# Optimization experiments

Measured on AMD Instinct MI355X. Metric: run time of the kernel, lower is better.

## Reference

```python
import jax, jax.numpy as jnp
from jax import lax
import numpy as np

T, B, I, H = 365, 2048, 9, 50


def setup_inputs() -> dict:
    key = jax.random.key(0)
    ks = jax.random.split(key, 12)
    s = 0.1
    return {
        "x": jax.random.normal(ks[0], (T, B, I), dtype=jnp.float32),
        "w_ih0": jax.random.normal(ks[1], (4 * H, I), dtype=jnp.float32) * s,
        "w_hh0": jax.random.normal(ks[2], (4 * H, H), dtype=jnp.float32) * s,
        "b_ih0": jax.random.normal(ks[3], (4 * H,), dtype=jnp.float32) * s,
        "b_hh0": jax.random.normal(ks[4], (4 * H,), dtype=jnp.float32) * s,
        "w_ih1": jax.random.normal(ks[5], (4 * H, H), dtype=jnp.float32) * s,
        "w_hh1": jax.random.normal(ks[6], (4 * H, H), dtype=jnp.float32) * s,
        "b_ih1": jax.random.normal(ks[7], (4 * H,), dtype=jnp.float32) * s,
        "b_hh1": jax.random.normal(ks[8], (4 * H,), dtype=jnp.float32) * s,
        "fc_w": jax.random.normal(ks[9], (1, H), dtype=jnp.float32) * s,
        "fc_b": jax.random.normal(ks[10], (1,), dtype=jnp.float32) * s,
    }


def _lstm_layer(x, w_ih, w_hh, b_ih, b_hh):
    # x: [T, B, in]; PyTorch gate order: i, f, g, o
    Bq = x.shape[1]
    Hh = w_hh.shape[1]
    # precompute input projections for all timesteps (one big GEMM)
    x_proj = jnp.einsum('tbi,gi->tbg', x, w_ih) + b_ih + b_hh  # [T, B, 4H]

    def step(carry, xp):
        h, c = carry
        gates = xp + h @ w_hh.T  # [B, 4H]
        i, f, g, o = jnp.split(gates, 4, axis=-1)
        i = jax.nn.sigmoid(i)
        f = jax.nn.sigmoid(f)
        g = jnp.tanh(g)
        o = jax.nn.sigmoid(o)
        c = f * c + i * g
        h = o * jnp.tanh(c)
        return (h, c), h

    h0 = jnp.zeros((Bq, Hh), dtype=x.dtype)
    _, hs = lax.scan(step, (h0, h0), x_proj)
    return hs  # [T, B, H]


def reference(x, w_ih0, w_hh0, b_ih0, b_hh0, w_ih1, w_hh1, b_ih1, b_hh1, fc_w, fc_b):
    h1 = _lstm_layer(x, w_ih0, w_hh0, b_ih0, b_hh0)
    h2 = _lstm_layer(h1, w_ih1, w_hh1, b_ih1, b_hh1)
    out = jnp.einsum('tbh,oh->tbo', h2, fc_w) + fc_b  # [T, B, 1]
    return out
```

## Files before the change

### kernel.cpp

```cpp
#include <hip/hip_runtime.h>

#define T_STEPS 365
#define BATCH   2048
#define INP     9
#define HID     50
#define MB      16
#define NBLK    (BATCH/MB)
#define NT      896
#define NWC     13
#define L2E     1.4426950408889634f

typedef __attribute__((ext_vector_type(8))) short short8;
typedef __attribute__((ext_vector_type(4))) float float4v;

__device__ __forceinline__ unsigned f2bf(float v) {
    unsigned u = __builtin_bit_cast(unsigned, v);
    return (u + 0x7FFFu + ((u >> 16) & 1u)) >> 16;
}

#define PHASE_BARRIER() do {                                  \
    asm volatile("s_waitcnt lgkmcnt(0)" ::: "memory");        \
    __builtin_amdgcn_s_barrier();                             \
    __builtin_amdgcn_sched_barrier(0);                        \
} while (0)

__device__ __forceinline__ int hx_off(int m, int k) {
    return (m * 128 + k) ^ ((m & 7) << 3);
}

__global__ __launch_bounds__(NT, 3)
void lstm_merged(const float* __restrict__ x,
                 const float* __restrict__ w_ih0, const float* __restrict__ w_hh0,
                 const float* __restrict__ b_ih0, const float* __restrict__ b_hh0,
                 const float* __restrict__ w_ih1, const float* __restrict__ w_hh1,
                 const float* __restrict__ b_ih1, const float* __restrict__ b_hh1,
                 const float* __restrict__ fc_w, const float* __restrict__ fc_b,
                 float* __restrict__ out)
{
    __shared__ __align__(16) unsigned short HX[2][MB * 128];
    __shared__ float FCP[2][NWC][MB];

    const int tid  = threadIdx.x;
    const int w    = tid >> 6;
    const int lid  = tid & 63;
    const int mcol = lid & 15;
    const int kgrp = lid >> 4;
    const int kb8  = kgrp * 8;
    const int b0   = blockIdx.x * MB;
    const bool cw  = (w < NWC);
    const float fcb = fc_b[0];

    const int T = cw ? w : 0;
    const int r = T * 16 + mcol;
    const bool rv = cw && (r < 4 * HID);
    const int u_r = r >> 2, g_r = r & 3;
    const int orig = g_r * HID + u_r;
    const float rsc = (g_r == 2) ? (-2.f * L2E) : (-L2E);
    const int u = T * 4 + kgrp;

    short8 wk0[2], wk1[2], wk2[2];
    #pragma unroll
    for (int q = 0; q < 2; ++q) {
        short8 a{}, b{}, c{};
        #pragma unroll
        for (int j = 0; j < 8; ++j) {
            const int k = q * 32 + kb8 + j;
            float v0 = 0.f, v1 = 0.f, v2 = 0.f;
            if (rv) {
                if (k < HID) {
                    v0 = w_hh0[orig * HID + k];
                    v1 = w_ih1[orig * HID + k];
                    v2 = w_hh1[orig * HID + k];
                } else if (k < HID + INP) {
                    v0 = w_ih0[orig * INP + (k - HID)];
                }
            }
            a[j] = (short)f2bf(v0 * rsc);
            b[j] = (short)f2bf(v1 * rsc);
            c[j] = (short)f2bf(v2 * rsc);
        }
        wk0[q] = a; wk1[q] = b; wk2[q] = c;
    }
    float bs0[4], bs1[4];
    #pragma unroll
    for (int rr = 0; rr < 4; ++rr) {
        const int row = T * 16 + kgrp * 4 + rr;
        const bool bv = cw && (row < 4 * HID);
        const float bsc = (rr == 2) ? (-2.f * L2E) : (-L2E);
        bs0[rr] = bv ? (b_ih0[rr * HID + u] + b_hh0[rr * HID + u]) * bsc : 0.f;
        bs1[rr] = bv ? (b_ih1[rr * HID + u] + b_hh1[rr * HID + u]) * bsc : 0.f;
    }
    const float fcwv = (cw && u < HID) ? fc_w[u] : 0.f;
    float cst0 = 0.f, cst1 = 0.f;

    const bool xact = (!cw) && (lid < 48);
    const bool oact = (!cw) && (lid >= 48);
    const int om = lid - 48;
    float xr[3] = {0.f, 0.f, 0.f};

    for (int i = tid; i < 2 * MB * 128; i += NT) (&HX[0][0])[i] = 0;
    for (int i = tid; i < 2 * NWC * MB; i += NT) (&FCP[0][0][0])[i] = 0.f;
    __syncthreads();
    if (xact) {
        #pragma unroll
        for (int q = 0; q < 3; ++q) {
            const int xi = lid * 3 + q;
            if (xi < MB * INP) {
                const int m = xi / INP, j = xi - m * INP;
                HX[1][hx_off(m, HID + j)] =
                    (unsigned short)f2bf(x[(size_t)(b0 + m) * INP + j]);
                xr[q] = x[((size_t)BATCH + b0 + m) * INP + j];
            }
        }
    }
    __syncthreads();

    for (int ph = 0; ph <= T_STEPS + 1; ++ph) {
        const int cur = (ph + 1) & 1, nxt = ph & 1;

        if (cw) {
            const short8 f0 = *(const short8*)&HX[cur][hx_off(mcol, kb8)];
            const short8 f1 = *(const short8*)&HX[cur][hx_off(mcol, 32 + kb8)];
            const short8 f2 = *(const short8*)&HX[cur][hx_off(mcol, 64 + kb8)];
            const short8 f3 = *(const short8*)&HX[cur][hx_off(mcol, 96 + kb8)];

            if (ph < T_STEPS) {
                float4v acc = {bs0[0], bs0[1], bs0[2], bs0[3]};
                acc = __builtin_amdgcn_mfma_f32_16x16x32_bf16(wk0[0], f0, acc, 0, 0, 0);
                acc = __builtin_amdgcn_mfma_f32_16x16x32_bf16(wk0[1], f1, acc, 0, 0, 0);
                const float gi = __builtin_amdgcn_rcpf(1.f + __builtin_amdgcn_exp2f(acc[0]));
                const float gf = __builtin_amdgcn_rcpf(1.f + __builtin_amdgcn_exp2f(acc[1]));
                const float g2 = __builtin_amdgcn_rcpf(1.f + __builtin_amdgcn_exp2f(acc[2]));
                const float go = __builtin_amdgcn_rcpf(1.f + __builtin_amdgcn_exp2f(acc[3]));
                const float gg = __builtin_fmaf(2.f, g2, -1.f);
                cst0 = gf * cst0 + gi * gg;
                const float Ec = __builtin_amdgcn_exp2f(cst0 * (-2.f * L2E));
                const float tc = __builtin_fmaf(2.f, __builtin_amdgcn_rcpf(1.f + Ec), -1.f);
                const float h0v = go * tc;
                if (u < HID) HX[nxt][hx_off(mcol, u)] = (unsigned short)f2bf(h0v);
            }

            if (ph >= 1 && ph <= T_STEPS) {
                float4v accA = {bs1[0], bs1[1], bs1[2], bs1[3]};
                float4v accB = {0.f, 0.f, 0.f, 0.f};
                accA = __builtin_amdgcn_mfma_f32_16x16x32_bf16(wk1[0], f0, accA, 0, 0, 0);
                accB = __builtin_amdgcn_mfma_f32_16x16x32_bf16(wk2[0], f2, accB, 0, 0, 0);
                accA = __builtin_amdgcn_mfma_f32_16x16x32_bf16(wk1[1], f1, accA, 0, 0, 0);
                accB = __builtin_amdgcn_mfma_f32_16x16x32_bf16(wk2[1], f3, accB, 0, 0, 0);
                const float gi = __builtin_amdgcn_rcpf(1.f + __builtin_amdgcn_exp2f(accA[0] + accB[0]));
                const float gf = __builtin_amdgcn_rcpf(1.f + __builtin_amdgcn_exp2f(accA[1] + accB[1]));
                const float g2 = __builtin_amdgcn_rcpf(1.f + __builtin_amdgcn_exp2f(accA[2] + accB[2]));
                const float go = __builtin_amdgcn_rcpf(1.f + __builtin_amdgcn_exp2f(accA[3] + accB[3]));
                const float gg = __builtin_fmaf(2.f, g2, -1.f);
                cst1 = gf * cst1 + gi * gg;
                const float Ec = __builtin_amdgcn_exp2f(cst1 * (-2.f * L2E));
                const float tc = __builtin_fmaf(2.f, __builtin_amdgcn_rcpf(1.f + Ec), -1.f);
                const float h1v = go * tc;
                if (u < HID) HX[nxt][hx_off(mcol, 64 + u)] = (unsigned short)f2bf(h1v);
                float fcp = fcwv * h1v;
                fcp += __shfl_xor(fcp, 16);
                fcp += __shfl_xor(fcp, 32);
                if (lid < MB) FCP[ph & 1][w][lid] = fcp;
            }
        } else if (xact) {
            #pragma unroll
            for (int q = 0; q < 3; ++q) {
                const int xi = lid * 3 + q;
                if (xi < MB * INP) {
                    const int m = xi / INP, j = xi - m * INP;
                    float xn = 0.f;
                    if (ph + 2 < T_STEPS)
                        xn = x[((size_t)(ph + 2) * BATCH + b0 + m) * INP + j];
                    if (ph + 1 < T_STEPS)
                        HX[nxt][hx_off(m, HID + j)] = (unsigned short)f2bf(xr[q]);
                    xr[q] = xn;
                }
            }
        } else if (oact && ph >= 2) {
            const int rp = (ph - 1) & 1;
            float s = fcb;
            #pragma unroll
            for (int vv = 0; vv < NWC; ++vv) s += FCP[rp][vv][om];
            out[(size_t)(ph - 2) * BATCH + b0 + om] = s;
        }
        PHASE_BARRIER();
    }
}

extern "C" void kernel_launch(void* const* d_in, const int* in_sizes, int n_in,
                              void* d_out, int out_size, void* d_ws, size_t ws_size,
                              hipStream_t stream) {
    const float* x     = (const float*)d_in[0];
    const float* w_ih0 = (const float*)d_in[1];
    const float* w_hh0 = (const float*)d_in[2];
    const float* b_ih0 = (const float*)d_in[3];
    const float* b_hh0 = (const float*)d_in[4];
    const float* w_ih1 = (const float*)d_in[5];
    const float* w_hh1 = (const float*)d_in[6];
    const float* b_ih1 = (const float*)d_in[7];
    const float* b_hh1 = (const float*)d_in[8];
    const float* fc_w  = (const float*)d_in[9];
    const float* fc_b  = (const float*)d_in[10];
    float* out = (float*)d_out;

    lstm_merged<<<dim3(NBLK), dim3(NT), 0, stream>>>(
        x, w_ih0, w_hh0, b_ih0, b_hh0,
        w_ih1, w_hh1, b_ih1, b_hh1, fc_w, fc_b, out);
}
```

Measured before the change: 333.8 us.

## Give each compute wave two gate tiles and fold FC head into MFMA

Cuts the block from 14 to 8 waves, with each compute wave handling two of the 13 gate tiles. The FC output is folded into an otherwise unused row of the last tile's layer-1 weight matrix, which removes the FCP shared buffer and the reduction waves. It also changes the LDS layout to a k-blocked transposed form and merges the sigmoid/tanh reciprocals in the cell update. Fewer waves may make barriers cheaper, but each wave now does twice the serial work per step, and the FC output is produced in bf16 precision.

```diff
diff --git a/kernel.cpp b/kernel.cpp
--- a/kernel.cpp
+++ b/kernel.cpp
@@ -6,8 +6,9 @@
 #define HID     50
 #define MB      16
 #define NBLK    (BATCH/MB)
-#define NT      896
-#define NWC     13
+#define NT      512
+#define NWC     7
+#define NTILES  13
 #define L2E     1.4426950408889634f
 
 typedef __attribute__((ext_vector_type(8))) short short8;
@@ -24,21 +25,32 @@
     __builtin_amdgcn_sched_barrier(0);                        \
 } while (0)
 
-__device__ __forceinline__ int hx_off(int m, int k) {
-    return (m * 128 + k) ^ ((m & 7) << 3);
-}
-
-__global__ __launch_bounds__(NT, 3)
-void lstm_merged(const float* __restrict__ x,
-                 const float* __restrict__ w_ih0, const float* __restrict__ w_hh0,
-                 const float* __restrict__ b_ih0, const float* __restrict__ b_hh0,
-                 const float* __restrict__ w_ih1, const float* __restrict__ w_hh1,
-                 const float* __restrict__ b_ih1, const float* __restrict__ b_hh1,
-                 const float* __restrict__ fc_w, const float* __restrict__ fc_b,
-                 float* __restrict__ out)
+__device__ __forceinline__ int tx_off(int m, int k) {
+    return ((k >> 3) * 128) + m * 8 + (k & 7);
+}
+
+__device__ __forceinline__ float cell_(float a0, float a1, float a2, float a3,
+                                       float& c) {
+    const float Ei = __builtin_amdgcn_exp2f(a0);
+    const float Ef = __builtin_amdgcn_exp2f(a1);
+    const float Eg = __builtin_amdgcn_exp2f(a2);
+    const float Eo = __builtin_amdgcn_exp2f(a3);
+    const float ig = (1.f - Eg) * __builtin_amdgcn_rcpf((1.f + Ei) * (1.f + Eg));
+    c = __builtin_amdgcn_rcpf(1.f + Ef) * c + ig;
+    const float Ec = __builtin_amdgcn_exp2f(c * (-2.f * L2E));
+    return (1.f - Ec) * __builtin_amdgcn_rcpf((1.f + Eo) * (1.f + Ec));
+}
+
+__global__ __launch_bounds__(NT, 2)
+void lstm_fuse8(const float* __restrict__ x,
+                const float* __restrict__ w_ih0, const float* __restrict__ w_hh0,
+                const float* __restrict__ b_ih0, const float* __restrict__ b_hh0,
+                const float* __restrict__ w_ih1, const float* __restrict__ w_hh1,
+                const float* __restrict__ b_ih1, const float* __restrict__ b_hh1,
+                const float* __restrict__ fc_w, const float* __restrict__ fc_b,
+                float* __restrict__ out)
 {
-    __shared__ __align__(16) unsigned short HX[2][MB * 128];
-    __shared__ float FCP[2][NWC][MB];
+    __shared__ __align__(16) unsigned short HX[2][2048];
 
     const int tid  = threadIdx.x;
     const int w    = tid >> 6;
@@ -48,58 +60,60 @@
     const int kb8  = kgrp * 8;
     const int b0   = blockIdx.x * MB;
     const bool cw  = (w < NWC);
-    const float fcb = fc_b[0];
-
-    const int T = cw ? w : 0;
-    const int r = T * 16 + mcol;
-    const bool rv = cw && (r < 4 * HID);
-    const int u_r = r >> 2, g_r = r & 3;
-    const int orig = g_r * HID + u_r;
-    const float rsc = (g_r == 2) ? (-2.f * L2E) : (-L2E);
-    const int u = T * 4 + kgrp;
-
-    short8 wk0[2], wk1[2], wk2[2];
+
+    short8 wk0[2][2], wk1[2][2], wk2[2][2];
+    float  bs0[2][4], bs1[2][4];
+    float  cst0[2] = {0.f, 0.f}, cst1[2] = {0.f, 0.f};
+
     #pragma unroll
-    for (int q = 0; q < 2; ++q) {
-        short8 a{}, b{}, c{};
+    for (int tt = 0; tt < 2; ++tt) {
+        const int T  = w + NWC * tt;
+        const bool tv = cw && (T < NTILES);
+        const int r  = T * 16 + mcol;
+        const bool rv = tv && (r < 4 * HID);
+        const int u_r = r >> 2, g_r = r & 3;
+        const int orig = g_r * HID + u_r;
+        const float rsc = (g_r == 2) ? (-2.f * L2E) : (-L2E);
+        const bool fcrow = tv && (T == 12) && (mcol == 8);
         #pragma unroll
-        for (int j = 0; j < 8; ++j) {
-            const int k = q * 32 + kb8 + j;
-            float v0 = 0.f, v1 = 0.f, v2 = 0.f;
-            if (rv) {
-                if (k < HID) {
-                    v0 = w_hh0[orig * HID + k];
-                    v1 = w_ih1[orig * HID + k];
-                    v2 = w_hh1[orig * HID + k];
-                } else if (k < HID + INP) {
-                    v0 = w_ih0[orig * INP + (k - HID)];
-                }
-            }
-            a[j] = (short)f2bf(v0 * rsc);
-            b[j] = (short)f2bf(v1 * rsc);
-            c[j] = (short)f2bf(v2 * rsc);
-        }
-        wk0[q] = a; wk1[q] = b; wk2[q] = c;
+        for (int q = 0; q < 2; ++q) {
+            short8 a{}, b{}, c{};
+            #pragma unroll
+            for (int j = 0; j < 8; ++j) {
+                const int k = q * 32 + kb8 + j;
+                float v0 = 0.f, v1 = 0.f, v2 = 0.f;
+                if (rv) {
+                    if (k < HID) {
+                        v0 = w_hh0[orig * HID + k] * rsc;
+                        v1 = w_ih1[orig * HID + k] * rsc;
+                        v2 = w_hh1[orig * HID + k] * rsc;
+                    } else if (k < HID + INP) {
+                        v0 = w_ih0[orig * INP + (k - HID)] * rsc;
+                    }
+                }
+                if (fcrow) v2 = (k < HID) ? fc_w[k] : 0.f;
+                a[j] = (short)f2bf(v0);
+                b[j] = (short)f2bf(v1);
+                c[j] = (short)f2bf(v2);
+            }
+            wk0[tt][q] = a; wk1[tt][q] = b; wk2[tt][q] = c;
+        }
+        #pragma unroll
+        for (int rr = 0; rr < 4; ++rr) {
+            const int row = T * 16 + kgrp * 4 + rr;
+            const bool bv = tv && (row < 4 * HID);
+            const int uu = row >> 2;
+            const float bsc = (rr == 2) ? (-2.f * L2E) : (-L2E);
+            bs0[tt][rr] = bv ? (b_ih0[rr * HID + uu] + b_hh0[rr * HID + uu]) * bsc : 0.f;
+            bs1[tt][rr] = bv ? (b_ih1[rr * HID + uu] + b_hh1[rr * HID + uu]) * bsc : 0.f;
+            if (tv && row == 4 * HID) bs1[tt][rr] = fc_b[0];
+        }
     }
-    float bs0[4], bs1[4];
-    #pragma unroll
-    for (int rr = 0; rr < 4; ++rr) {
-        const int row = T * 16 + kgrp * 4 + rr;
-        const bool bv = cw && (row < 4 * HID);
-        const float bsc = (rr == 2) ? (-2.f * L2E) : (-L2E);
-        bs0[rr] = bv ? (b_ih0[rr * HID + u] + b_hh0[rr * HID + u]) * bsc : 0.f;
-        bs1[rr] = bv ? (b_ih1[rr * HID + u] + b_hh1[rr * HID + u]) * bsc : 0.f;
-    }
-    const float fcwv = (cw && u < HID) ? fc_w[u] : 0.f;
-    float cst0 = 0.f, cst1 = 0.f;
 
     const bool xact = (!cw) && (lid < 48);
-    const bool oact = (!cw) && (lid >= 48);
-    const int om = lid - 48;
     float xr[3] = {0.f, 0.f, 0.f};
 
-    for (int i = tid; i < 2 * MB * 128; i += NT) (&HX[0][0])[i] = 0;
-    for (int i = tid; i < 2 * NWC * MB; i += NT) (&FCP[0][0][0])[i] = 0.f;
+    for (int i = tid; i < 2 * 2048; i += NT) (&HX[0][0])[i] = 0;
     __syncthreads();
     if (xact) {
         #pragma unroll
@@ -107,7 +121,7 @@
             const int xi = lid * 3 + q;
             if (xi < MB * INP) {
                 const int m = xi / INP, j = xi - m * INP;
-                HX[1][hx_off(m, HID + j)] =
+                HX[1][tx_off(m, HID + j)] =
                     (unsigned short)f2bf(x[(size_t)(b0 + m) * INP + j]);
                 xr[q] = x[((size_t)BATCH + b0 + m) * INP + j];
             }
@@ -119,48 +133,44 @@
         const int cur = (ph + 1) & 1, nxt = ph & 1;
 
         if (cw) {
-            const short8 f0 = *(const short8*)&HX[cur][hx_off(mcol, kb8)];
-            const short8 f1 = *(const short8*)&HX[cur][hx_off(mcol, 32 + kb8)];
-            const short8 f2 = *(const short8*)&HX[cur][hx_off(mcol, 64 + kb8)];
-            const short8 f3 = *(const short8*)&HX[cur][hx_off(mcol, 96 + kb8)];
-
-            if (ph < T_STEPS) {
-                float4v acc = {bs0[0], bs0[1], bs0[2], bs0[3]};
-                acc = __builtin_amdgcn_mfma_f32_16x16x32_bf16(wk0[0], f0, acc, 0, 0, 0);
-                acc = __builtin_amdgcn_mfma_f32_16x16x32_bf16(wk0[1], f1, acc, 0, 0, 0);
-                const float gi = __builtin_amdgcn_rcpf(1.f + __builtin_amdgcn_exp2f(acc[0]));
-                const float gf = __builtin_amdgcn_rcpf(1.f + __builtin_amdgcn_exp2f(acc[1]));
-                const float g2 = __builtin_amdgcn_rcpf(1.f + __builtin_amdgcn_exp2f(acc[2]));
-                const float go = __builtin_amdgcn_rcpf(1.f + __builtin_amdgcn_exp2f(acc[3]));
-                const float gg = __builtin_fmaf(2.f, g2, -1.f);
-                cst0 = gf * cst0 + gi * gg;
-                const float Ec = __builtin_amdgcn_exp2f(cst0 * (-2.f * L2E));
-                const float tc = __builtin_fmaf(2.f, __builtin_amdgcn_rcpf(1.f + Ec), -1.f);
-                const float h0v = go * tc;
-                if (u < HID) HX[nxt][hx_off(mcol, u)] = (unsigned short)f2bf(h0v);
-            }
-
-            if (ph >= 1 && ph <= T_STEPS) {
-                float4v accA = {bs1[0], bs1[1], bs1[2], bs1[3]};
-                float4v accB = {0.f, 0.f, 0.f, 0.f};
-                accA = __builtin_amdgcn_mfma_f32_16x16x32_bf16(wk1[0], f0, accA, 0, 0, 0);
-                accB = __builtin_amdgcn_mfma_f32_16x16x32_bf16(wk2[0], f2, accB, 0, 0, 0);
-                accA = __builtin_amdgcn_mfma_f32_16x16x32_bf16(wk1[1], f1, accA, 0, 0, 0);
-                accB = __builtin_amdgcn_mfma_f32_16x16x32_bf16(wk2[1], f3, accB, 0, 0, 0);
-                const float gi = __builtin_amdgcn_rcpf(1.f + __builtin_amdgcn_exp2f(accA[0] + accB[0]));
-                const float gf = __builtin_amdgcn_rcpf(1.f + __builtin_amdgcn_exp2f(accA[1] + accB[1]));
-                const float g2 = __builtin_amdgcn_rcpf(1.f + __builtin_amdgcn_exp2f(accA[2] + accB[2]));
-                const float go = __builtin_amdgcn_rcpf(1.f + __builtin_amdgcn_exp2f(accA[3] + accB[3]));
-                const float gg = __builtin_fmaf(2.f, g2, -1.f);
-                cst1 = gf * cst1 + gi * gg;
-                const float Ec = __builtin_amdgcn_exp2f(cst1 * (-2.f * L2E));
-                const float tc = __builtin_fmaf(2.f, __builtin_amdgcn_rcpf(1.f + Ec), -1.f);
-                const float h1v = go * tc;
-                if (u < HID) HX[nxt][hx_off(mcol, 64 + u)] = (unsigned short)f2bf(h1v);
-                float fcp = fcwv * h1v;
-                fcp += __shfl_xor(fcp, 16);
-                fcp += __shfl_xor(fcp, 32);
-                if (lid < MB) FCP[ph & 1][w][lid] = fcp;
+            const int base = mcol * 8;
+            const short8 f0 = *(const short8*)&HX[cur][(kgrp)      * 128 + base];
+            const short8 f1 = *(const short8*)&HX[cur][(4  + kgrp) * 128 + base];
+            const short8 f2 = *(const short8*)&HX[cur][(8  + kgrp) * 128 + base];
+            const short8 f3 = *(const short8*)&HX[cur][(12 + kgrp) * 128 + base];
+
+            #pragma unroll
+            for (int tt = 0; tt < 2; ++tt) {
+                const int T = w + NWC * tt;
+                if (T >= NTILES) continue;
+                const int u = T * 4 + kgrp;
+
+                if (ph < T_STEPS) {
+                    float4v acc = {bs0[tt][0], bs0[tt][1], bs0[tt][2], bs0[tt][3]};
+                    acc = __builtin_amdgcn_mfma_f32_16x16x32_bf16(wk0[tt][0], f0, acc, 0, 0, 0);
+                    acc = __builtin_amdgcn_mfma_f32_16x16x32_bf16(wk0[tt][1], f1, acc, 0, 0, 0);
+                    const float h0v = cell_(acc[0], acc[1], acc[2], acc[3], cst0[tt]);
+                    if (u < HID) HX[nxt][tx_off(mcol, u)] = (unsigned short)f2bf(h0v);
+                }
+
+                if (ph >= 1) {
+                    float4v accA = {bs1[tt][0], bs1[tt][1], bs1[tt][2], bs1[tt][3]};
+                    float4v accB = {0.f, 0.f, 0.f, 0.f};
+                    accA = __builtin_amdgcn_mfma_f32_16x16x32_bf16(wk1[tt][0], f0, accA, 0, 0, 0);
+                    accB = __builtin_amdgcn_mfma_f32_16x16x32_bf16(wk2[tt][0], f2, accB, 0, 0, 0);
+                    accA = __builtin_amdgcn_mfma_f32_16x16x32_bf16(wk1[tt][1], f1, accA, 0, 0, 0);
+                    accB = __builtin_amdgcn_mfma_f32_16x16x32_bf16(wk2[tt][1], f3, accB, 0, 0, 0);
+                    const float a0 = accA[0] + accB[0];
+                    const float a1 = accA[1] + accB[1];
+                    const float a2 = accA[2] + accB[2];
+                    const float a3 = accA[3] + accB[3];
+                    if (T == 12 && kgrp == 2 && ph >= 2)
+                        out[(size_t)(ph - 2) * BATCH + b0 + mcol] = a0;
+                    if (ph <= T_STEPS) {
+                        const float h1v = cell_(a0, a1, a2, a3, cst1[tt]);
+                        if (u < HID) HX[nxt][tx_off(mcol, 64 + u)] = (unsigned short)f2bf(h1v);
+                    }
+                }
             }
         } else if (xact) {
             #pragma unroll
@@ -172,16 +182,10 @@
                     if (ph + 2 < T_STEPS)
                         xn = x[((size_t)(ph + 2) * BATCH + b0 + m) * INP + j];
                     if (ph + 1 < T_STEPS)
-                        HX[nxt][hx_off(m, HID + j)] = (unsigned short)f2bf(xr[q]);
+                        HX[nxt][tx_off(m, HID + j)] = (unsigned short)f2bf(xr[q]);
                     xr[q] = xn;
                 }
             }
-        } else if (oact && ph >= 2) {
-            const int rp = (ph - 1) & 1;
-            float s = fcb;
-            #pragma unroll
-            for (int vv = 0; vv < NWC; ++vv) s += FCP[rp][vv][om];
-            out[(size_t)(ph - 2) * BATCH + b0 + om] = s;
         }
         PHASE_BARRIER();
     }
@@ -203,7 +207,7 @@
     const float* fc_b  = (const float*)d_in[10];
     float* out = (float*)d_out;
 
-    lstm_merged<<<dim3(NBLK), dim3(NT), 0, stream>>>(
+    lstm_fuse8<<<dim3(NBLK), dim3(NT), 0, stream>>>(
         x, w_ih0, w_hh0, b_ih0, b_hh0,
         w_ih1, w_hh1, b_ih1, b_hh1, fc_w, fc_b, out);
 }
```

Result: no change. 335.6 us (+0.6%).
